# Kernel tuning notes

Measured on AMD Instinct MI355X. Metric: run time of the kernel, lower is better.

Reference implementation:

```python
import jax, jax.numpy as jnp
import numpy as np

L, B, D = 512, 32, 256  # seq_len, batch (hardcoded 32 in source), in_size == hidden_size
H = D


def setup_inputs() -> dict:
    key = jax.random.key(0)
    ks = jax.random.split(key, 9)
    s_in = 1.0 / np.sqrt(D)
    s_h = 1.0 / np.sqrt(H)
    return {
        "v": jax.random.normal(ks[0], (L, B, D), jnp.float32),
        "h0": jax.random.normal(ks[1], (B, H), jnp.float32),       # torch.randn h
        "Vvec": jax.random.normal(ks[2], (B, H), jnp.float32),     # torch.randn V (squeezed [B,H,1])
        "Wp": jax.random.normal(ks[3], (H, D), jnp.float32) * s_in,   # nn.Linear(D,H,bias=False).weight
        "Wp_": jax.random.normal(ks[4], (H, D), jnp.float32) * s_in,
        "W_ih": jax.random.normal(ks[5], (3 * H, D), jnp.float32) * s_h,  # GRUCell weight_ih
        "W_hh": jax.random.normal(ks[6], (3 * H, H), jnp.float32) * s_h,
        "b_ih": jax.random.normal(ks[7], (3 * H,), jnp.float32) * s_h,
        "b_hh": jax.random.normal(ks[8], (3 * H,), jnp.float32) * s_h,
    }


def _gru_cell(c, h, W_ih, W_hh, b_ih, b_hh):
    # torch.nn.GRUCell math
    gi = c @ W_ih.T + b_ih   # [B, 3H]
    gh = h @ W_hh.T + b_hh   # [B, 3H]
    i_r, i_z, i_n = jnp.split(gi, 3, axis=1)
    h_r, h_z, h_n = jnp.split(gh, 3, axis=1)
    r = jax.nn.sigmoid(i_r + h_r)
    z = jax.nn.sigmoid(i_z + h_z)
    n = jnp.tanh(i_n + r * h_n)
    return (1.0 - z) * n + z * h


def reference(v, h0, Vvec, Wp, Wp_, W_ih, W_hh, b_ih, b_hh):
    # Hoist the two linear projections out of the scan (they don't depend on h).
    xq = jnp.einsum('lbd,hd->lbh', v, Wp)    # Wp(v[i]) for all i
    xv = jnp.einsum('lbd,hd->lbh', v, Wp_)   # Wp_(v), reused every step

    def step(h, xq_i):
        x = jnp.tanh(xq_i[None, :, :] + xv)          # [L, B, H]
        s = jnp.einsum('lbh,bh->bl', x, Vvec)        # attention scores over L
        a = jax.nn.softmax(s, axis=1)                # [B, L]
        c = jnp.einsum('bl,lbd->bd', a, v)           # context [B, D]
        h_new = _gru_cell(c, h, W_ih, W_hh, b_ih, b_hh)
        return h_new, h_new

    _, hs = jax.lax.scan(step, h0, xq)  # hs: [L, B, H]
    # dropout is identity in eval mode
    return hs
```

## Files before the change

### kernel.cpp

```cpp
#include <hip/hip_runtime.h>
#include <stdint.h>


#define C2    2.8853900817779268f
#define LOG2E 1.4426950408889634f

typedef __fp16 f16x2 __attribute__((ext_vector_type(2)));
typedef __fp16 f16x4_t __attribute__((ext_vector_type(4)));
typedef __fp16 f16x8 __attribute__((ext_vector_type(8)));
typedef float f32x4 __attribute__((ext_vector_type(4)));

static __device__ __forceinline__ float rcp_f(float x)  { return __builtin_amdgcn_rcpf(x); }
static __device__ __forceinline__ float exp2_f(float x) { return __builtin_amdgcn_exp2f(x); }
#if __has_builtin(__builtin_amdgcn_rcph)
static __device__ __forceinline__ __fp16 rcph(__fp16 x) {
  return (__fp16)__builtin_amdgcn_rcph((_Float16)x);
}
#else
static __device__ __forceinline__ __fp16 rcph(__fp16 x) {
  return (__fp16)__builtin_amdgcn_rcpf((float)x);
}
#endif
static __device__ __forceinline__ float dot2f(f16x2 a, f16x2 b, float c) {
  return __builtin_amdgcn_fdot2(a, b, c, false);
}
static __device__ __forceinline__ f16x8 cvt8(float4 a, float4 b) {
  f16x8 f;
  f[0] = (__fp16)a.x; f[1] = (__fp16)a.y; f[2] = (__fp16)a.z; f[3] = (__fp16)a.w;
  f[4] = (__fp16)b.x; f[5] = (__fp16)b.y; f[6] = (__fp16)b.z; f[7] = (__fp16)b.w;
  return f;
}


__global__ __launch_bounds__(256) void proj_k(
    const float* __restrict__ v, const float* __restrict__ Wp,
    const float* __restrict__ Wp_, __fp16* __restrict__ Eq,
    __fp16* __restrict__ Ev)
{
  __shared__ __align__(16) __fp16 As[64][40];
  __shared__ __align__(16) __fp16 Wqs[64][40];
  __shared__ __align__(16) __fp16 Wvs[64][40];
  const int t = threadIdx.x, wave = t >> 6, lane = t & 63;
  const int quad = lane >> 4, col = lane & 15;
  const int n0 = blockIdx.x * 64, m0 = blockIdx.y * 64;
  const int srow = t >> 2, skq = t & 3;

  f32x4 accq[4], accv[4];
#pragma unroll
  for (int nt = 0; nt < 4; ++nt) {
    accq[nt] = (f32x4){0.f, 0.f, 0.f, 0.f};
    accv[nt] = (f32x4){0.f, 0.f, 0.f, 0.f};
  }

  for (int kc = 0; kc < 8; ++kc) {
    const int k0 = kc * 32;
    {
      const float4* ap = (const float4*)&v[(size_t)(m0 + srow) * 256 + k0 + skq * 8];
      *(f16x8*)&As[srow][skq * 8] = cvt8(ap[0], ap[1]);
      const float4* qp = (const float4*)&Wp[(size_t)(n0 + srow) * 256 + k0 + skq * 8];
      *(f16x8*)&Wqs[srow][skq * 8] = cvt8(qp[0], qp[1]);
      const float4* vp = (const float4*)&Wp_[(size_t)(n0 + srow) * 256 + k0 + skq * 8];
      *(f16x8*)&Wvs[srow][skq * 8] = cvt8(vp[0], vp[1]);
    }
    __syncthreads();
    f16x8 a = *(const f16x8*)&As[wave * 16 + col][quad * 8];
#pragma unroll
    for (int nt = 0; nt < 4; ++nt) {
      f16x8 bq = *(const f16x8*)&Wqs[nt * 16 + col][quad * 8];
      f16x8 bv = *(const f16x8*)&Wvs[nt * 16 + col][quad * 8];
      accq[nt] = __builtin_amdgcn_mfma_f32_16x16x32_f16(a, bq, accq[nt], 0, 0, 0);
      accv[nt] = __builtin_amdgcn_mfma_f32_16x16x32_f16(a, bv, accv[nt], 0, 0, 0);
    }
    __syncthreads();
  }

#pragma unroll
  for (int nt = 0; nt < 4; ++nt)
#pragma unroll
    for (int r = 0; r < 4; ++r) {
      size_t m = m0 + wave * 16 + quad * 4 + r;
      size_t n = n0 + nt * 16 + col;
      float eq = C2 * accq[nt][r], ev = C2 * accv[nt][r];
      eq = fminf(fmaxf(eq, -14.f), 15.5f);
      ev = fminf(fmaxf(ev, -14.f), 15.5f);
      Eq[m * 256 + n] = (__fp16)exp2_f(eq);
      Ev[m * 256 + n] = (__fp16)exp2_f(ev);
    }
}

__global__ __launch_bounds__(256) void vt_k(
    const float* __restrict__ v, __fp16* __restrict__ VT)
{
  __shared__ float Ts[32][33];
  const int t = threadIdx.x;
  const int d0 = blockIdx.x * 32, l0 = blockIdx.y * 32, b = blockIdx.z;
  {
    int lrow = t >> 3, dq = t & 7;
    float4 a = *(const float4*)&v[((size_t)(l0 + lrow) * 32 + b) * 256 + d0 + dq * 4];
    Ts[dq * 4 + 0][lrow] = a.x; Ts[dq * 4 + 1][lrow] = a.y;
    Ts[dq * 4 + 2][lrow] = a.z; Ts[dq * 4 + 3][lrow] = a.w;
  }
  __syncthreads();
  {
    int drow = t >> 3, lq = t & 7;
    f16x4_t o;
#pragma unroll
    for (int e = 0; e < 4; ++e) o[e] = (__fp16)Ts[drow][lq * 4 + e];
    *(f16x4_t*)&VT[((size_t)b * 256 + d0 + drow) * 512 + l0 + lq * 4] = o;
  }
}

__global__ __launch_bounds__(256) void score_k(
    const __fp16* __restrict__ Eq, const __fp16* __restrict__ Ev,
    const float* __restrict__ Vvec, float* __restrict__ S)
{
  __shared__ __align__(16) __fp16 Eqs[64][72];
  __shared__ __align__(16) __fp16 Evs[32][72];
  __shared__ __align__(16) __fp16 Vs[256];
  const int t = threadIdx.x;
  const int tx = t & 15, ty = t >> 4;
  const int l0 = blockIdx.x * 32;
  const int i0 = blockIdx.y * 64;
  const int b  = blockIdx.z;

  Vs[t] = (__fp16)(-2.0f * Vvec[b * 256 + t]);
  float acc[4][2] = {};
  const f16x2 one2 = {(__fp16)1.f, (__fp16)1.f};

  for (int st = 0; st < 4; ++st) {
    const int h0 = st * 64;
#pragma unroll
    for (int s = 0; s < 2; ++s) {
      int f = t + s * 256;
      int row = f >> 3, cq = f & 7;
      *(f16x8*)&Eqs[row][cq * 8] =
          *(const f16x8*)&Eq[((size_t)(i0 + row) * 32 + b) * 256 + h0 + cq * 8];
    }
    {
      int row = t >> 3, cq = t & 7;
      *(f16x8*)&Evs[row][cq * 8] =
          *(const f16x8*)&Ev[((size_t)(l0 + row) * 32 + b) * 256 + h0 + cq * 8];
    }
    __syncthreads();

#pragma unroll
    for (int k8 = 0; k8 < 8; ++k8) {
      f16x8 vh8 = *(const f16x8*)&Vs[h0 + k8 * 8];
      f16x8 ev80 = *(const f16x8*)&Evs[tx][k8 * 8];
      f16x8 ev81 = *(const f16x8*)&Evs[tx + 16][k8 * 8];
      f16x8 eq8[4];
#pragma unroll
      for (int r = 0; r < 4; ++r)
        eq8[r] = *(const f16x8*)&Eqs[ty * 4 + r][k8 * 8];
#pragma unroll
      for (int q = 0; q < 4; ++q) {
        f16x2 vh2 = {vh8[q * 2], vh8[q * 2 + 1]};
        f16x2 e0  = {ev80[q * 2], ev80[q * 2 + 1]};
        f16x2 e1  = {ev81[q * 2], ev81[q * 2 + 1]};
#pragma unroll
        for (int r = 0; r < 4; ++r) {
          f16x2 eq2 = {eq8[r][q * 2], eq8[r][q * 2 + 1]};
          f16x2 d0 = eq2 * e0 + one2;
          f16x2 d1 = eq2 * e1 + one2;
          f16x2 r0 = {rcph(d0[0]), rcph(d0[1])};
          f16x2 r1 = {rcph(d1[0]), rcph(d1[1])};
          acc[r][0] = dot2f(vh2, r0, acc[r][0]);
          acc[r][1] = dot2f(vh2, r1, acc[r][1]);
        }
      }
    }
    __syncthreads();
  }

#pragma unroll
  for (int r = 0; r < 4; ++r) {
    float* ps = &S[((size_t)b * 512 + i0 + ty * 4 + r) * 512 + l0];
    ps[tx]      = acc[r][0];
    ps[tx + 16] = acc[r][1];
  }
}

__global__ __launch_bounds__(256) void softmax_k(float* __restrict__ S)
{
  const int wave = threadIdx.x >> 6, lane = threadIdx.x & 63;
  float* row = &S[((size_t)blockIdx.x * 4 + wave) * 512];
  float4 x0 = *(float4*)&row[lane * 4];
  float4 x1 = *(float4*)&row[256 + lane * 4];
  float m = fmaxf(fmaxf(fmaxf(x0.x, x0.y), fmaxf(x0.z, x0.w)),
                  fmaxf(fmaxf(x1.x, x1.y), fmaxf(x1.z, x1.w)));
#pragma unroll
  for (int o = 32; o; o >>= 1) m = fmaxf(m, __shfl_xor(m, o, 64));
  x0.x = exp2_f(LOG2E * (x0.x - m)); x0.y = exp2_f(LOG2E * (x0.y - m));
  x0.z = exp2_f(LOG2E * (x0.z - m)); x0.w = exp2_f(LOG2E * (x0.w - m));
  x1.x = exp2_f(LOG2E * (x1.x - m)); x1.y = exp2_f(LOG2E * (x1.y - m));
  x1.z = exp2_f(LOG2E * (x1.z - m)); x1.w = exp2_f(LOG2E * (x1.w - m));
  float sum = x0.x + x0.y + x0.z + x0.w + x1.x + x1.y + x1.z + x1.w;
#pragma unroll
  for (int o = 32; o; o >>= 1) sum += __shfl_xor(sum, o, 64);
  float inv = rcp_f(sum);
  x0.x *= inv; x0.y *= inv; x0.z *= inv; x0.w *= inv;
  x1.x *= inv; x1.y *= inv; x1.z *= inv; x1.w *= inv;
  *(float4*)&row[lane * 4] = x0;
  *(float4*)&row[256 + lane * 4] = x1;
}

__global__ __launch_bounds__(256) void ctxm_k(
    const float* __restrict__ Aw, const __fp16* __restrict__ VT,
    float* __restrict__ C)
{
  __shared__ __align__(16) __fp16 As[64][40];
  __shared__ __align__(16) __fp16 Vs[64][40];
  const int t = threadIdx.x, wave = t >> 6, lane = t & 63;
  const int quad = lane >> 4, col = lane & 15;
  const int d0 = blockIdx.x * 64, i0 = blockIdx.y * 64, b = blockIdx.z;
  const int srow = t >> 2, skq = t & 3;

  f32x4 acc[4];
#pragma unroll
  for (int nt = 0; nt < 4; ++nt) acc[nt] = (f32x4){0.f, 0.f, 0.f, 0.f};

  for (int kc = 0; kc < 16; ++kc) {
    const int l0 = kc * 32;
    {
      const float4* ap =
          (const float4*)&Aw[((size_t)b * 512 + i0 + srow) * 512 + l0 + skq * 8];
      *(f16x8*)&As[srow][skq * 8] = cvt8(ap[0], ap[1]);
      *(f16x8*)&Vs[srow][skq * 8] =
          *(const f16x8*)&VT[((size_t)b * 256 + d0 + srow) * 512 + l0 + skq * 8];
    }
    __syncthreads();
    f16x8 a = *(const f16x8*)&As[wave * 16 + col][quad * 8];
#pragma unroll
    for (int nt = 0; nt < 4; ++nt) {
      f16x8 bb = *(const f16x8*)&Vs[nt * 16 + col][quad * 8];
      acc[nt] = __builtin_amdgcn_mfma_f32_16x16x32_f16(a, bb, acc[nt], 0, 0, 0);
    }
    __syncthreads();
  }

#pragma unroll
  for (int nt = 0; nt < 4; ++nt)
#pragma unroll
    for (int r = 0; r < 4; ++r) {
      size_t i = i0 + wave * 16 + quad * 4 + r;
      size_t d = d0 + nt * 16 + col;
      C[(i * 32 + b) * 256 + d] = acc[nt][r];
    }
}

__global__ __launch_bounds__(256) void gi_k(
    const float* __restrict__ A, const float* __restrict__ W,
    const float* __restrict__ bih, const float* __restrict__ bhh,
    __fp16* __restrict__ G)
{
  __shared__ __align__(16) __fp16 As[64][40];
  __shared__ __align__(16) __fp16 Ws[64][40];
  const int t = threadIdx.x, wave = t >> 6, lane = t & 63;
  const int quad = lane >> 4, col = lane & 15;
  const int n0 = blockIdx.x * 64, m0 = blockIdx.y * 64;
  const int srow = t >> 2, skq = t & 3;

  f32x4 acc[4];
#pragma unroll
  for (int nt = 0; nt < 4; ++nt) acc[nt] = (f32x4){0.f, 0.f, 0.f, 0.f};

  for (int kc = 0; kc < 8; ++kc) {
    const int k0 = kc * 32;
    {
      const float4* ap = (const float4*)&A[(size_t)(m0 + srow) * 256 + k0 + skq * 8];
      *(f16x8*)&As[srow][skq * 8] = cvt8(ap[0], ap[1]);
      const float4* wp = (const float4*)&W[(size_t)(n0 + srow) * 256 + k0 + skq * 8];
      *(f16x8*)&Ws[srow][skq * 8] = cvt8(wp[0], wp[1]);
    }
    __syncthreads();
    f16x8 a = *(const f16x8*)&As[wave * 16 + col][quad * 8];
#pragma unroll
    for (int nt = 0; nt < 4; ++nt) {
      f16x8 b = *(const f16x8*)&Ws[nt * 16 + col][quad * 8];
      acc[nt] = __builtin_amdgcn_mfma_f32_16x16x32_f16(a, b, acc[nt], 0, 0, 0);
    }
    __syncthreads();
  }

#pragma unroll
  for (int nt = 0; nt < 4; ++nt) {
    int n = n0 + nt * 16 + col;
    float bias = bih[n] + (n < 512 ? bhh[n] : 0.f);
#pragma unroll
    for (int r = 0; r < 4; ++r) {
      size_t m = m0 + wave * 16 + quad * 4 + r;
      G[m * 768 + n] = (__fp16)(acc[nt][r] + bias);
    }
  }
}

__global__ __launch_bounds__(512, 1) void gru_k(
    const __fp16* __restrict__ Gi2, const float* __restrict__ Whh,
    const float* __restrict__ bhh, const float* __restrict__ h0,
    float* __restrict__ out)
{
  __shared__ __align__(16) __fp16 hA[2][256];
  const int t = threadIdx.x, wave = t >> 6, lane = t & 63;
  const int quad = lane >> 4, col = lane & 15;
  const int b = blockIdx.x;
  const int jw = wave * 32;

  f16x8 Bf[2][3][8];
#pragma unroll
  for (int p = 0; p < 2; ++p)
#pragma unroll
    for (int g = 0; g < 3; ++g) {
      const float* wrow = &Whh[(size_t)(g * 256 + jw + p * 16 + col) * 256];
#pragma unroll
      for (int kk = 0; kk < 8; ++kk) {
        const float4* wp = (const float4*)&wrow[kk * 32 + quad * 8];
        Bf[p][g][kk] = cvt8(wp[0], wp[1]);
      }
    }

  float hold[2];
  float bn[2];
#pragma unroll
  for (int p = 0; p < 2; ++p) {
    int j = jw + p * 16 + col;
    bn[p] = bhh[512 + j];
    float h = h0[(size_t)b * 256 + j];
    hold[p] = h;
    if (quad == 0) hA[0][j] = (__fp16)h;
  }
  __syncthreads();

  __fp16 gcur[2][3];
#pragma unroll
  for (int p = 0; p < 2; ++p)
#pragma unroll
    for (int g = 0; g < 3; ++g)
      gcur[p][g] = Gi2[(size_t)b * 768 + g * 256 + jw + p * 16 + col];

  for (int i = 0; i < 512; ++i) {
    __fp16 gnext[2][3];
    {
      int ip = (i + 1 < 512) ? (i + 1) : 511;
#pragma unroll
      for (int p = 0; p < 2; ++p)
#pragma unroll
        for (int g = 0; g < 3; ++g)
          gnext[p][g] =
              Gi2[(size_t)(ip * 32 + b) * 768 + g * 256 + jw + p * 16 + col];
    }

    f32x4 acc[2][3];
#pragma unroll
    for (int p = 0; p < 2; ++p)
#pragma unroll
      for (int g = 0; g < 3; ++g)
        acc[p][g] = (f32x4){0.f, 0.f, 0.f, 0.f};

    const __fp16* hbuf = hA[i & 1];
#pragma unroll
    for (int kk = 0; kk < 8; ++kk) {
      f16x8 a = *(const f16x8*)&hbuf[kk * 32 + quad * 8];
#pragma unroll
      for (int p = 0; p < 2; ++p)
#pragma unroll
        for (int g = 0; g < 3; ++g)
          acc[p][g] = __builtin_amdgcn_mfma_f32_16x16x32_f16(
              a, Bf[p][g][kk], acc[p][g], 0, 0, 0);
    }

    __fp16* hnext = hA[(i + 1) & 1];
#pragma unroll
    for (int p = 0; p < 2; ++p) {
      int j = jw + p * 16 + col;
      float rr = rcp_f(1.f + exp2_f(-LOG2E * ((float)gcur[p][0] + acc[p][0][0])));
      float zz = rcp_f(1.f + exp2_f(-LOG2E * ((float)gcur[p][1] + acc[p][1][0])));
      float na = fmaf(rr, acc[p][2][0] + bn[p], (float)gcur[p][2]);
      float nn = fmaf(-2.f, rcp_f(1.f + exp2_f(C2 * na)), 1.f);
      float h = fmaf(zz, hold[p] - nn, nn);
      hold[p] = h;
      if (quad == 0) {
        out[((size_t)i * 32 + b) * 256 + j] = h;
        hnext[j] = (__fp16)h;
      }
    }
#pragma unroll
    for (int p = 0; p < 2; ++p)
#pragma unroll
      for (int g = 0; g < 3; ++g) gcur[p][g] = gnext[p][g];
    __syncthreads();
  }
}

extern "C" void kernel_launch(void* const* d_in, const int* in_sizes, int n_in,
                              void* d_out, int out_size, void* d_ws, size_t ws_size,
                              hipStream_t stream)
{
  const float* v   = (const float*)d_in[0];
  const float* h0  = (const float*)d_in[1];
  const float* Vv  = (const float*)d_in[2];
  const float* Wp  = (const float*)d_in[3];
  const float* Wp_ = (const float*)d_in[4];
  const float* Wih = (const float*)d_in[5];
  const float* Whh = (const float*)d_in[6];
  const float* bih = (const float*)d_in[7];
  const float* bhh = (const float*)d_in[8];
  float* out = (float*)d_out;
  float* ws  = (float*)d_ws;

  __fp16* Eq  = (__fp16*)ws;
  __fp16* Ev  = (__fp16*)(ws + 2097152);
  __fp16* VT  = (__fp16*)(ws + 4194304);
  float*  S   = ws + 6291456;
  float*  C   = ws;
  __fp16* Gi2 = (__fp16*)(ws + 6291456);

  proj_k<<<dim3(4, 256), 256, 0, stream>>>(v, Wp, Wp_, Eq, Ev);
  vt_k<<<dim3(8, 16, 32), 256, 0, stream>>>(v, VT);
  score_k<<<dim3(16, 8, 32), 256, 0, stream>>>(Eq, Ev, Vv, S);
  softmax_k<<<4096, 256, 0, stream>>>(S);
  ctxm_k<<<dim3(4, 8, 32), 256, 0, stream>>>(S, VT, C);
  gi_k<<<dim3(12, 256), 256, 0, stream>>>(C, Wih, bih, bhh, Gi2);
  gru_k<<<32, 512, 0, stream>>>(Gi2, Whh, bhh, h0, out);
}
```

Measured before the change: 923.2 us.

## Fuse softmax into context matmul kernel with full-D tiles per block

Removes the separate softmax kernel and instead computes row max and sum inside the context kernel, then normalizes scores on the fly while staging them into shared memory as fp16. Each block now covers all 256 output columns with 512 threads, so the scores are read once per block instead of once per 64-column tile. This drops the softmax write-back and one launch, at the cost of reading the score rows three times inside the fused kernel and a much smaller grid (256 blocks versus 1024).

```diff
diff --git a/kernel.cpp b/kernel.cpp
--- a/kernel.cpp
+++ b/kernel.cpp
@@ -180,71 +180,97 @@
   }
 }
 
-__global__ __launch_bounds__(256) void softmax_k(float* __restrict__ S)
-{
-  const int wave = threadIdx.x >> 6, lane = threadIdx.x & 63;
-  float* row = &S[((size_t)blockIdx.x * 4 + wave) * 512];
-  float4 x0 = *(float4*)&row[lane * 4];
-  float4 x1 = *(float4*)&row[256 + lane * 4];
-  float m = fmaxf(fmaxf(fmaxf(x0.x, x0.y), fmaxf(x0.z, x0.w)),
-                  fmaxf(fmaxf(x1.x, x1.y), fmaxf(x1.z, x1.w)));
-#pragma unroll
-  for (int o = 32; o; o >>= 1) m = fmaxf(m, __shfl_xor(m, o, 64));
-  x0.x = exp2_f(LOG2E * (x0.x - m)); x0.y = exp2_f(LOG2E * (x0.y - m));
-  x0.z = exp2_f(LOG2E * (x0.z - m)); x0.w = exp2_f(LOG2E * (x0.w - m));
-  x1.x = exp2_f(LOG2E * (x1.x - m)); x1.y = exp2_f(LOG2E * (x1.y - m));
-  x1.z = exp2_f(LOG2E * (x1.z - m)); x1.w = exp2_f(LOG2E * (x1.w - m));
-  float sum = x0.x + x0.y + x0.z + x0.w + x1.x + x1.y + x1.z + x1.w;
-#pragma unroll
-  for (int o = 32; o; o >>= 1) sum += __shfl_xor(sum, o, 64);
-  float inv = rcp_f(sum);
-  x0.x *= inv; x0.y *= inv; x0.z *= inv; x0.w *= inv;
-  x1.x *= inv; x1.y *= inv; x1.z *= inv; x1.w *= inv;
-  *(float4*)&row[lane * 4] = x0;
-  *(float4*)&row[256 + lane * 4] = x1;
-}
-
-__global__ __launch_bounds__(256) void ctxm_k(
-    const float* __restrict__ Aw, const __fp16* __restrict__ VT,
+__global__ __launch_bounds__(512) void ctxsm_k(
+    const float* __restrict__ S, const __fp16* __restrict__ VT,
     float* __restrict__ C)
 {
   __shared__ __align__(16) __fp16 As[64][40];
-  __shared__ __align__(16) __fp16 Vs[64][40];
+  __shared__ __align__(16) __fp16 Vs[256][40];
+  __shared__ float red[64][8];
+  __shared__ float stat_m[64], stat_inv[64];
   const int t = threadIdx.x, wave = t >> 6, lane = t & 63;
   const int quad = lane >> 4, col = lane & 15;
-  const int d0 = blockIdx.x * 64, i0 = blockIdx.y * 64, b = blockIdx.z;
-  const int srow = t >> 2, skq = t & 3;
-
-  f32x4 acc[4];
-#pragma unroll
-  for (int nt = 0; nt < 4; ++nt) acc[nt] = (f32x4){0.f, 0.f, 0.f, 0.f};
+  const int i0 = blockIdx.x * 64, b = blockIdx.y;
+  const int mt = wave & 3, nh = wave >> 2;
+
+  {
+    const int row = t >> 3, seg = t & 7;
+    const float* sp = &S[((size_t)b * 512 + i0 + row) * 512 + seg * 64];
+    float m = -1e30f;
+#pragma unroll
+    for (int u = 0; u < 16; ++u) {
+      float4 x = *(const float4*)&sp[u * 4];
+      m = fmaxf(m, fmaxf(fmaxf(x.x, x.y), fmaxf(x.z, x.w)));
+    }
+    red[row][seg] = m;
+    __syncthreads();
+    if (seg == 0) {
+      float mm = red[row][0];
+#pragma unroll
+      for (int u = 1; u < 8; ++u) mm = fmaxf(mm, red[row][u]);
+      stat_m[row] = mm;
+    }
+    __syncthreads();
+    float M = stat_m[row];
+    float s = 0.f;
+#pragma unroll
+    for (int u = 0; u < 16; ++u) {
+      float4 x = *(const float4*)&sp[u * 4];
+      s += exp2_f(LOG2E * (x.x - M)) + exp2_f(LOG2E * (x.y - M)) +
+           exp2_f(LOG2E * (x.z - M)) + exp2_f(LOG2E * (x.w - M));
+    }
+    red[row][seg] = s;
+    __syncthreads();
+    if (seg == 0) {
+      float ss = red[row][0];
+#pragma unroll
+      for (int u = 1; u < 8; ++u) ss += red[row][u];
+      stat_inv[row] = rcp_f(ss);
+    }
+    __syncthreads();
+  }
+
+  f32x4 acc[8];
+#pragma unroll
+  for (int n = 0; n < 8; ++n) acc[n] = (f32x4){0.f, 0.f, 0.f, 0.f};
 
   for (int kc = 0; kc < 16; ++kc) {
     const int l0 = kc * 32;
     {
-      const float4* ap =
-          (const float4*)&Aw[((size_t)b * 512 + i0 + srow) * 512 + l0 + skq * 8];
-      *(f16x8*)&As[srow][skq * 8] = cvt8(ap[0], ap[1]);
-      *(f16x8*)&Vs[srow][skq * 8] =
-          *(const f16x8*)&VT[((size_t)b * 256 + d0 + srow) * 512 + l0 + skq * 8];
-    }
-    __syncthreads();
-    f16x8 a = *(const f16x8*)&As[wave * 16 + col][quad * 8];
-#pragma unroll
-    for (int nt = 0; nt < 4; ++nt) {
-      f16x8 bb = *(const f16x8*)&Vs[nt * 16 + col][quad * 8];
-      acc[nt] = __builtin_amdgcn_mfma_f32_16x16x32_f16(a, bb, acc[nt], 0, 0, 0);
-    }
-    __syncthreads();
-  }
-
-#pragma unroll
-  for (int nt = 0; nt < 4; ++nt)
+      int arow = t >> 3, aq = t & 7;
+      float M = stat_m[arow], inv = stat_inv[arow];
+      float4 x = *(const float4*)&S[((size_t)b * 512 + i0 + arow) * 512 + l0 + aq * 4];
+      f16x4_t o;
+      o[0] = (__fp16)(exp2_f(LOG2E * (x.x - M)) * inv);
+      o[1] = (__fp16)(exp2_f(LOG2E * (x.y - M)) * inv);
+      o[2] = (__fp16)(exp2_f(LOG2E * (x.z - M)) * inv);
+      o[3] = (__fp16)(exp2_f(LOG2E * (x.w - M)) * inv);
+      *(f16x4_t*)&As[arow][aq * 4] = o;
+#pragma unroll
+      for (int s2 = 0; s2 < 2; ++s2) {
+        int f = t + s2 * 512;
+        int vrow = f >> 2, vq = f & 3;
+        *(f16x8*)&Vs[vrow][vq * 8] =
+            *(const f16x8*)&VT[((size_t)b * 256 + vrow) * 512 + l0 + vq * 8];
+      }
+    }
+    __syncthreads();
+    f16x8 a = *(const f16x8*)&As[mt * 16 + col][quad * 8];
+#pragma unroll
+    for (int n = 0; n < 8; ++n) {
+      f16x8 vf = *(const f16x8*)&Vs[nh * 128 + n * 16 + col][quad * 8];
+      acc[n] = __builtin_amdgcn_mfma_f32_16x16x32_f16(a, vf, acc[n], 0, 0, 0);
+    }
+    __syncthreads();
+  }
+
+#pragma unroll
+  for (int n = 0; n < 8; ++n)
 #pragma unroll
     for (int r = 0; r < 4; ++r) {
-      size_t i = i0 + wave * 16 + quad * 4 + r;
-      size_t d = d0 + nt * 16 + col;
-      C[(i * 32 + b) * 256 + d] = acc[nt][r];
+      size_t i = i0 + mt * 16 + quad * 4 + r;
+      size_t d = nh * 128 + n * 16 + col;
+      C[(i * 32 + b) * 256 + d] = acc[n][r];
     }
 }
 
@@ -417,8 +443,7 @@
   proj_k<<<dim3(4, 256), 256, 0, stream>>>(v, Wp, Wp_, Eq, Ev);
   vt_k<<<dim3(8, 16, 32), 256, 0, stream>>>(v, VT);
   score_k<<<dim3(16, 8, 32), 256, 0, stream>>>(Eq, Ev, Vv, S);
-  softmax_k<<<4096, 256, 0, stream>>>(S);
-  ctxm_k<<<dim3(4, 8, 32), 256, 0, stream>>>(S, VT, C);
+  ctxsm_k<<<dim3(8, 32), 512, 0, stream>>>(S, VT, C);
   gi_k<<<dim3(12, 256), 256, 0, stream>>>(C, Wih, bih, bhh, Gi2);
   gru_k<<<32, 512, 0, stream>>>(Gi2, Whh, bhh, h0, out);
 }
```

Result: no change. 919.1 us (median of 2 runs) (-0.4%).
